# Performance work log

Measured on AMD Instinct MI355X. Metric: run time of the kernel, lower is better.

Reference implementation:

```python
import jax, jax.numpy as jnp
import numpy as np

B, D, OUT = 8192, 1024, 256
H1, H2 = 8, 4
EPS = 1e-5


def setup_inputs() -> dict:
    key = jax.random.key(0)
    ks = jax.random.split(key, 8)
    sc = lambda k, shape: jax.random.normal(k, shape, jnp.float32) * 0.05
    return {
        "x": jax.random.normal(ks[0], (B, D), jnp.float32),
        "W1": sc(ks[1], (D, H1, 1)),      # D diagonal blocks of the masked Linear(D -> 8D)
        "b1": sc(ks[2], (D * H1,)),
        "g1": jnp.ones((D * H1,), jnp.float32),
        "be1": jnp.zeros((D * H1,), jnp.float32),
        "W2": sc(ks[3], (D, H2, H1)),     # D diagonal blocks of the masked Linear(8D -> 4D)
        "b2": sc(ks[4], (D * H2,)),
        "g2": jnp.ones((D * H2,), jnp.float32),
        "be2": jnp.zeros((D * H2,), jnp.float32),
        "Wfc": sc(ks[5], (OUT, D * H2)),
        "bfc": sc(ks[6], (OUT,)),
    }


def _batchnorm(h, g, b):
    # BatchNorm1d in training mode: per-channel batch mean, biased variance
    mu = h.mean(axis=0)
    var = h.var(axis=0)  # ddof=0 (biased), matching torch normalization
    return g * (h - mu) * jax.lax.rsqrt(var + EPS) + b


def reference(x, W1, b1, g1, be1, W2, b2, g2, be2, Wfc, bfc):
    n = x.shape[0]
    # layer 1: per-feature (1 -> H1) block GEMM == masked dense Linear
    h = jnp.einsum("bdi,doi->bdo", x[:, :, None], W1).reshape(n, D * H1)
    h = jax.nn.relu(_batchnorm(h + b1, g1, be1))
    # layer 2: per-feature (H1 -> H2) block GEMM
    h = jnp.einsum("bdi,doi->bdo", h.reshape(n, D, H1), W2).reshape(n, D * H2)
    h = jax.nn.relu(_batchnorm(h + b2, g2, be2))
    # dense output head
    return h @ Wfc.T + bfc
```

## Files before the change

kernel.cpp:

```cpp
#include <hip/hip_runtime.h>

#define EPSV 1e-5f

typedef short bf16x8 __attribute__((ext_vector_type(8)));
typedef float f32x4 __attribute__((ext_vector_type(4)));

static __device__ __forceinline__ unsigned short f2b(float f) {
  union { float f; unsigned u; } v; v.f = f;
  return (unsigned short)((v.u + 0x7fffu + ((v.u >> 16) & 1u)) >> 16);
}

__global__ void k_pre(const float* __restrict__ wfc, unsigned short* __restrict__ wb,
                      const float* __restrict__ x, float* __restrict__ ps1) {
  if (blockIdx.x < 512) {
    const int f = blockIdx.x * 256 + threadIdx.x;
    const int l15 = f & 15, quad = (f >> 4) & 3, nb = (f >> 6) & 15, k32b = f >> 10;
    const int n = nb * 16 + l15;
    const int k = k32b * 32 + quad * 8;
    const float4* src = (const float4*)(wfc + (size_t)n * 4096 + k);
    float4 a = src[0], b = src[1];
    ushort4 o0, o1;
    o0.x = f2b(a.x); o0.y = f2b(a.y); o0.z = f2b(a.z); o0.w = f2b(a.w);
    o1.x = f2b(b.x); o1.y = f2b(b.y); o1.z = f2b(b.z); o1.w = f2b(b.w);
    *(ushort4*)(wb + (size_t)f * 8) = o0;
    *(ushort4*)(wb + (size_t)f * 8 + 4) = o1;
  } else {
    const int blk = blockIdx.x - 512;
    const int c = threadIdx.x * 4;
    const int r0 = blk * 32;
    float4 s = {0.f,0.f,0.f,0.f}, q = {0.f,0.f,0.f,0.f};
    for (int g = 0; g < 4; ++g) {
      float4 v[8];
#pragma unroll
      for (int j = 0; j < 8; ++j)
        v[j] = *(const float4*)(x + (size_t)(r0 + g*8 + j) * 1024 + c);
#pragma unroll
      for (int j = 0; j < 8; ++j) {
        s.x += v[j].x; s.y += v[j].y; s.z += v[j].z; s.w += v[j].w;
        q.x = fmaf(v[j].x, v[j].x, q.x); q.y = fmaf(v[j].y, v[j].y, q.y);
        q.z = fmaf(v[j].z, v[j].z, q.z); q.w = fmaf(v[j].w, v[j].w, q.w);
      }
    }
    *(float4*)(ps1 + (size_t)blk * 2048 + c) = s;
    *(float4*)(ps1 + (size_t)blk * 2048 + 1024 + c) = q;
  }
}

__global__ __launch_bounds__(256) void k_fin1(const float* __restrict__ ps1,
    const float* __restrict__ W1, const float* __restrict__ g1,
    const float* __restrict__ be1, float* __restrict__ pt) {
  __shared__ float redS[8][32], redQ[8][32];
  const int t = threadIdx.x;
  const int d0 = blockIdx.x * 32;
  const int dl = t & 31, slot = t >> 5;
  float s = 0.f, q = 0.f;
  for (int u = 0; u < 32; u += 8) {
#pragma unroll
    for (int w = 0; w < 8; ++w) {
      const size_t base = (size_t)(slot * 32 + u + w) * 2048 + d0 + dl;
      s += ps1[base];
      q += ps1[base + 1024];
    }
  }
  redS[slot][dl] = s; redQ[slot][dl] = q;
  __syncthreads();
  const int dloc = t >> 3, i = t & 7;
  float xs = 0.f, xq = 0.f;
#pragma unroll
  for (int p = 0; p < 8; ++p) { xs += redS[p][dloc]; xq += redQ[p][dloc]; }
  const float inv = 1.f / 8192.f;
  const int d = d0 + dloc;
  const int c = d * 8 + i;
  float mean = xs * inv;
  float var = xq * inv - mean * mean;
  float w = W1[c];
  float s1 = g1[c] * w * rsqrtf(w * w * var + EPSV);
  float t1 = be1[c] - s1 * mean;
  pt[i * 1024 + d] = s1;
  pt[(8 + i) * 1024 + d] = t1;
}

__global__ __launch_bounds__(256) void k_stats2(const float* __restrict__ x,
    const float* __restrict__ pt, const float* __restrict__ W2,
    float* __restrict__ ps2s, float* __restrict__ ps2q) {
  __shared__ float red[8][32][8];
  const int t = threadIdx.x;
  const int dl = t & 31, slot = t >> 5;
  const int d = blockIdx.x * 32 + dl;
  float s1v[8], t1v[8], w2v[32];
#pragma unroll
  for (int i = 0; i < 8; ++i) s1v[i] = pt[i * 1024 + d];
#pragma unroll
  for (int i = 0; i < 8; ++i) t1v[i] = pt[(8 + i) * 1024 + d];
  const float4* wp = (const float4*)(W2 + (size_t)d * 32);
#pragma unroll
  for (int i = 0; i < 8; ++i) {
    float4 v = wp[i];
    w2v[i*4+0]=v.x; w2v[i*4+1]=v.y; w2v[i*4+2]=v.z; w2v[i*4+3]=v.w;
  }
  float s[4] = {0.f,0.f,0.f,0.f}, q[4] = {0.f,0.f,0.f,0.f};
  const int b0 = blockIdx.y * 256 + slot * 32;
  for (int r = 0; r < 32; r += 8) {
    float xv[8];
#pragma unroll
    for (int j = 0; j < 8; ++j)
      xv[j] = x[(size_t)(b0 + r + j) * 1024 + d];
#pragma unroll
    for (int j = 0; j < 8; ++j) {
      float a1[8];
#pragma unroll
      for (int i = 0; i < 8; ++i) a1[i] = fmaxf(fmaf(s1v[i], xv[j], t1v[i]), 0.f);
#pragma unroll
      for (int o = 0; o < 4; ++o) {
        float h = 0.f;
#pragma unroll
        for (int i = 0; i < 8; ++i) h = fmaf(a1[i], w2v[o*8+i], h);
        s[o] += h;
        q[o] = fmaf(h, h, q[o]);
      }
    }
  }
#pragma unroll
  for (int j = 0; j < 4; ++j) {
    red[slot][dl][j] = s[j];
    red[slot][dl][4+j] = q[j];
  }
  __syncthreads();
  const int d2l = t >> 3, j = t & 7;
  float v = 0.f;
#pragma unroll
  for (int p = 0; p < 8; ++p) v += red[p][d2l][j];
  const int c2 = (blockIdx.x * 32 + d2l) * 4 + (t & 3);
  if (j < 4) ps2s[(size_t)blockIdx.y * 4096 + c2] = v;
  else       ps2q[(size_t)blockIdx.y * 4096 + c2] = v;
}

__global__ void k_fin2(const float* __restrict__ W2, const float* __restrict__ g2,
                       const float* __restrict__ be2, const float* __restrict__ ps2s,
                       const float* __restrict__ ps2q, float* __restrict__ pt) {
  const int c2 = blockIdx.x * 256 + threadIdx.x;
  const int d = c2 >> 2, o = c2 & 3;
  float sm = 0.f, sq = 0.f;
#pragma unroll
  for (int b = 0; b < 32; ++b) {
    sm += ps2s[(size_t)b * 4096 + c2];
    sq += ps2q[(size_t)b * 4096 + c2];
  }
  const float inv = 1.f / 8192.f;
  float m = sm * inv;
  float var = sq * inv - m * m;
  float s2 = g2[c2] * rsqrtf(var + EPSV);
  float t2 = be2[c2] - s2 * m;
  pt[(48 + o) * 1024 + d] = t2;
#pragma unroll
  for (int i = 0; i < 8; ++i)
    pt[(16 + o * 8 + i) * 1024 + d] = W2[(size_t)d * 32 + o * 8 + i] * s2;
}

__global__ __launch_bounds__(256, 2) void k_gemm(const float* __restrict__ x,
    const float* __restrict__ pt, const unsigned short* __restrict__ wb,
    const float* __restrict__ bfc, float* __restrict__ out) {
  __shared__ __align__(16) unsigned short As[64 * 136];
  const int t = threadIdx.x;
  const int lane = t & 63;
  const int wv = t >> 6;
  const int m0 = blockIdx.x * 64;
  const int kQ = blockIdx.y;
  const int d0 = kQ * 256;
  const int quad = lane >> 4;
  const int l15 = lane & 15;
  const int dl = t & 31, bs = t >> 5;
  const int chrot = (blockIdx.x & 1) << 2;

  f32x4 acc[4][4];
#pragma unroll
  for (int mt = 0; mt < 4; ++mt)
#pragma unroll
    for (int nt = 0; nt < 4; ++nt) {
      f32x4 z = {0.f, 0.f, 0.f, 0.f};
      acc[mt][nt] = z;
    }

  for (int chi = 0; chi < 8; ++chi) {
    const int ch = (chi + chrot) & 7;
    const int d = d0 + ch * 32 + dl;
    float pv[52];
#pragma unroll
    for (int i = 0; i < 52; ++i) pv[i] = pt[i * 1024 + d];
    __syncthreads();
#pragma unroll
    for (int r = 0; r < 8; ++r) {
      const int bl = bs * 8 + r;
      float xv = x[(size_t)(m0 + bl) * 1024 + d];
      float a1[8];
#pragma unroll
      for (int i = 0; i < 8; ++i) a1[i] = fmaxf(fmaf(pv[i], xv, pv[8+i]), 0.f);
      unsigned short o4[4];
#pragma unroll
      for (int o = 0; o < 4; ++o) {
        float h = pv[48 + o];
#pragma unroll
        for (int i = 0; i < 8; ++i) h = fmaf(a1[i], pv[16 + o*8 + i], h);
        o4[o] = f2b(fmaxf(h, 0.f));
      }
      *(ushort4*)&As[bl * 136 + dl * 4] = make_ushort4(o4[0], o4[1], o4[2], o4[3]);
    }
    __syncthreads();
#pragma unroll
    for (int kk = 0; kk < 4; ++kk) {
      bf16x8 af[4];
#pragma unroll
      for (int mt = 0; mt < 4; ++mt)
        af[mt] = *(const bf16x8*)&As[(mt*16 + l15) * 136 + kk*32 + quad*8];
      const int k32b = kQ * 32 + ch * 4 + kk;
#pragma unroll
      for (int nt = 0; nt < 4; ++nt) {
        const int frag = k32b * 16 + wv * 4 + nt;
        bf16x8 bfr = *(const bf16x8*)&wb[((size_t)frag * 64 + lane) * 8];
#pragma unroll
        for (int mt = 0; mt < 4; ++mt)
          acc[mt][nt] = __builtin_amdgcn_mfma_f32_16x16x32_bf16(af[mt], bfr,
                                                                acc[mt][nt], 0, 0, 0);
      }
    }
  }
#pragma unroll
  for (int nt = 0; nt < 4; ++nt) {
    const int col = wv * 64 + nt * 16 + l15;
    const float bias = (kQ == 0) ? bfc[col] : 0.f;
#pragma unroll
    for (int mt = 0; mt < 4; ++mt) {
#pragma unroll
      for (int r = 0; r < 4; ++r) {
        const int row = m0 + mt * 16 + quad * 4 + r;
        atomicAdd(&out[(size_t)row * 256 + col], acc[mt][nt][r] + bias);
      }
    }
  }
}

extern "C" void kernel_launch(void* const* d_in, const int* in_sizes, int n_in,
                              void* d_out, int out_size, void* d_ws, size_t ws_size,
                              hipStream_t stream) {
  const float* x   = (const float*)d_in[0];
  const float* W1  = (const float*)d_in[1];
  const float* g1  = (const float*)d_in[3];
  const float* be1 = (const float*)d_in[4];
  const float* W2  = (const float*)d_in[5];
  const float* g2  = (const float*)d_in[7];
  const float* be2 = (const float*)d_in[8];
  const float* Wfc = (const float*)d_in[9];
  const float* bfc = (const float*)d_in[10];
  float* out = (float*)d_out;

  char* ws = (char*)d_ws;
  unsigned short* wb = (unsigned short*)ws;
  float* pt     = (float*)(ws + (2u << 20));
  float* shared = (float*)(ws + (2u << 20) + (256u << 10));
  float* ps1  = shared;
  float* ps2s = shared;
  float* ps2q = shared + 32 * 4096;

  hipMemsetAsync(d_out, 0, (size_t)out_size * sizeof(float), stream);

  k_pre   <<<dim3(768),    256, 0, stream>>>(Wfc, wb, x, ps1);
  k_fin1  <<<dim3(32),     256, 0, stream>>>(ps1, W1, g1, be1, pt);
  k_stats2<<<dim3(32, 32), 256, 0, stream>>>(x, pt, W2, ps2s, ps2q);
  k_fin2  <<<dim3(16),     256, 0, stream>>>(W2, g2, be2, ps2s, ps2q, pt);
  k_gemm  <<<dim3(128, 4), 256, 0, stream>>>(x, pt, wb, bfc, out);
}
```

Measured before the change: 187.0 us.

## Fuse all stages into one persistent kernel with grid-wide atomic barriers

New measurement: 410.8 us. 120% more time.

```diff
diff --git a/kernel.cpp b/kernel.cpp
--- a/kernel.cpp
+++ b/kernel.cpp
@@ -4,16 +4,47 @@
 
 typedef short bf16x8 __attribute__((ext_vector_type(8)));
 typedef float f32x4 __attribute__((ext_vector_type(4)));
+
+#define NBLK 512
 
 static __device__ __forceinline__ unsigned short f2b(float f) {
   union { float f; unsigned u; } v; v.f = f;
   return (unsigned short)((v.u + 0x7fffu + ((v.u >> 16) & 1u)) >> 16);
 }
 
-__global__ void k_pre(const float* __restrict__ wfc, unsigned short* __restrict__ wb,
-                      const float* __restrict__ x, float* __restrict__ ps1) {
-  if (blockIdx.x < 512) {
-    const int f = blockIdx.x * 256 + threadIdx.x;
+static __device__ __forceinline__ void gbar(int* bar) {
+  __syncthreads();
+  if (threadIdx.x == 0) {
+    __hip_atomic_fetch_add(bar, 1, __ATOMIC_ACQ_REL, __HIP_MEMORY_SCOPE_AGENT);
+    for (int it = 0; it < (1 << 27); ++it) {
+      if (__hip_atomic_load(bar, __ATOMIC_ACQUIRE, __HIP_MEMORY_SCOPE_AGENT) >= NBLK)
+        break;
+    }
+  }
+  __syncthreads();
+}
+
+__global__ __launch_bounds__(256, 2) void k_all(
+    const float* __restrict__ x, const float* __restrict__ W1,
+    const float* __restrict__ g1, const float* __restrict__ be1,
+    const float* __restrict__ W2, const float* __restrict__ g2,
+    const float* __restrict__ be2, const float* __restrict__ wfc,
+    const float* __restrict__ bfc, unsigned short* __restrict__ wb,
+    float* __restrict__ pt, float* __restrict__ ps1,
+    float* __restrict__ ps2s, float* __restrict__ ps2q,
+    int* __restrict__ bars, float* __restrict__ out) {
+  __shared__ __align__(16) unsigned char smem[64 * 136 * 2];
+  const int t = threadIdx.x;
+  const int blk = blockIdx.x;
+
+  {
+    const size_t gid = (size_t)blk * 256 + t;
+    float4 z4 = {0.f, 0.f, 0.f, 0.f};
+    float4* ob = (float4*)(out + gid * 16);
+#pragma unroll
+    for (int j = 0; j < 4; ++j) ob[j] = z4;
+
+    const int f = blk * 256 + t;
     const int l15 = f & 15, quad = (f >> 4) & 3, nb = (f >> 6) & 15, k32b = f >> 10;
     const int n = nb * 16 + l15;
     const int k = k32b * 32 + quad * 8;
@@ -24,216 +55,218 @@
     o1.x = f2b(b.x); o1.y = f2b(b.y); o1.z = f2b(b.z); o1.w = f2b(b.w);
     *(ushort4*)(wb + (size_t)f * 8) = o0;
     *(ushort4*)(wb + (size_t)f * 8 + 4) = o1;
-  } else {
-    const int blk = blockIdx.x - 512;
-    const int c = threadIdx.x * 4;
-    const int r0 = blk * 32;
-    float4 s = {0.f,0.f,0.f,0.f}, q = {0.f,0.f,0.f,0.f};
-    for (int g = 0; g < 4; ++g) {
-      float4 v[8];
-#pragma unroll
-      for (int j = 0; j < 8; ++j)
-        v[j] = *(const float4*)(x + (size_t)(r0 + g*8 + j) * 1024 + c);
-#pragma unroll
-      for (int j = 0; j < 8; ++j) {
-        s.x += v[j].x; s.y += v[j].y; s.z += v[j].z; s.w += v[j].w;
-        q.x = fmaf(v[j].x, v[j].x, q.x); q.y = fmaf(v[j].y, v[j].y, q.y);
-        q.z = fmaf(v[j].z, v[j].z, q.z); q.w = fmaf(v[j].w, v[j].w, q.w);
-      }
-    }
-    *(float4*)(ps1 + (size_t)blk * 2048 + c) = s;
-    *(float4*)(ps1 + (size_t)blk * 2048 + 1024 + c) = q;
-  }
-}
-
-__global__ __launch_bounds__(256) void k_fin1(const float* __restrict__ ps1,
-    const float* __restrict__ W1, const float* __restrict__ g1,
-    const float* __restrict__ be1, float* __restrict__ pt) {
-  __shared__ float redS[8][32], redQ[8][32];
-  const int t = threadIdx.x;
-  const int d0 = blockIdx.x * 32;
-  const int dl = t & 31, slot = t >> 5;
-  float s = 0.f, q = 0.f;
-  for (int u = 0; u < 32; u += 8) {
-#pragma unroll
-    for (int w = 0; w < 8; ++w) {
-      const size_t base = (size_t)(slot * 32 + u + w) * 2048 + d0 + dl;
-      s += ps1[base];
-      q += ps1[base + 1024];
-    }
-  }
-  redS[slot][dl] = s; redQ[slot][dl] = q;
-  __syncthreads();
-  const int dloc = t >> 3, i = t & 7;
-  float xs = 0.f, xq = 0.f;
-#pragma unroll
-  for (int p = 0; p < 8; ++p) { xs += redS[p][dloc]; xq += redQ[p][dloc]; }
-  const float inv = 1.f / 8192.f;
-  const int d = d0 + dloc;
-  const int c = d * 8 + i;
-  float mean = xs * inv;
-  float var = xq * inv - mean * mean;
-  float w = W1[c];
-  float s1 = g1[c] * w * rsqrtf(w * w * var + EPSV);
-  float t1 = be1[c] - s1 * mean;
-  pt[i * 1024 + d] = s1;
-  pt[(8 + i) * 1024 + d] = t1;
-}
-
-__global__ __launch_bounds__(256) void k_stats2(const float* __restrict__ x,
-    const float* __restrict__ pt, const float* __restrict__ W2,
-    float* __restrict__ ps2s, float* __restrict__ ps2q) {
-  __shared__ float red[8][32][8];
-  const int t = threadIdx.x;
-  const int dl = t & 31, slot = t >> 5;
-  const int d = blockIdx.x * 32 + dl;
-  float s1v[8], t1v[8], w2v[32];
-#pragma unroll
-  for (int i = 0; i < 8; ++i) s1v[i] = pt[i * 1024 + d];
-#pragma unroll
-  for (int i = 0; i < 8; ++i) t1v[i] = pt[(8 + i) * 1024 + d];
-  const float4* wp = (const float4*)(W2 + (size_t)d * 32);
-#pragma unroll
-  for (int i = 0; i < 8; ++i) {
-    float4 v = wp[i];
-    w2v[i*4+0]=v.x; w2v[i*4+1]=v.y; w2v[i*4+2]=v.z; w2v[i*4+3]=v.w;
-  }
-  float s[4] = {0.f,0.f,0.f,0.f}, q[4] = {0.f,0.f,0.f,0.f};
-  const int b0 = blockIdx.y * 256 + slot * 32;
-  for (int r = 0; r < 32; r += 8) {
-    float xv[8];
-#pragma unroll
-    for (int j = 0; j < 8; ++j)
-      xv[j] = x[(size_t)(b0 + r + j) * 1024 + d];
-#pragma unroll
-    for (int j = 0; j < 8; ++j) {
-      float a1[8];
-#pragma unroll
-      for (int i = 0; i < 8; ++i) a1[i] = fmaxf(fmaf(s1v[i], xv[j], t1v[i]), 0.f);
-#pragma unroll
-      for (int o = 0; o < 4; ++o) {
-        float h = 0.f;
-#pragma unroll
-        for (int i = 0; i < 8; ++i) h = fmaf(a1[i], w2v[o*8+i], h);
-        s[o] += h;
-        q[o] = fmaf(h, h, q[o]);
-      }
-    }
-  }
-#pragma unroll
-  for (int j = 0; j < 4; ++j) {
-    red[slot][dl][j] = s[j];
-    red[slot][dl][4+j] = q[j];
-  }
-  __syncthreads();
-  const int d2l = t >> 3, j = t & 7;
-  float v = 0.f;
-#pragma unroll
-  for (int p = 0; p < 8; ++p) v += red[p][d2l][j];
-  const int c2 = (blockIdx.x * 32 + d2l) * 4 + (t & 3);
-  if (j < 4) ps2s[(size_t)blockIdx.y * 4096 + c2] = v;
-  else       ps2q[(size_t)blockIdx.y * 4096 + c2] = v;
-}
-
-__global__ void k_fin2(const float* __restrict__ W2, const float* __restrict__ g2,
-                       const float* __restrict__ be2, const float* __restrict__ ps2s,
-                       const float* __restrict__ ps2q, float* __restrict__ pt) {
-  const int c2 = blockIdx.x * 256 + threadIdx.x;
-  const int d = c2 >> 2, o = c2 & 3;
-  float sm = 0.f, sq = 0.f;
-#pragma unroll
-  for (int b = 0; b < 32; ++b) {
-    sm += ps2s[(size_t)b * 4096 + c2];
-    sq += ps2q[(size_t)b * 4096 + c2];
-  }
-  const float inv = 1.f / 8192.f;
-  float m = sm * inv;
-  float var = sq * inv - m * m;
-  float s2 = g2[c2] * rsqrtf(var + EPSV);
-  float t2 = be2[c2] - s2 * m;
-  pt[(48 + o) * 1024 + d] = t2;
-#pragma unroll
-  for (int i = 0; i < 8; ++i)
-    pt[(16 + o * 8 + i) * 1024 + d] = W2[(size_t)d * 32 + o * 8 + i] * s2;
-}
-
-__global__ __launch_bounds__(256, 2) void k_gemm(const float* __restrict__ x,
-    const float* __restrict__ pt, const unsigned short* __restrict__ wb,
-    const float* __restrict__ bfc, float* __restrict__ out) {
-  __shared__ __align__(16) unsigned short As[64 * 136];
-  const int t = threadIdx.x;
-  const int lane = t & 63;
-  const int wv = t >> 6;
-  const int m0 = blockIdx.x * 64;
-  const int kQ = blockIdx.y;
-  const int d0 = kQ * 256;
-  const int quad = lane >> 4;
-  const int l15 = lane & 15;
-  const int dl = t & 31, bs = t >> 5;
-  const int chrot = (blockIdx.x & 1) << 2;
-
-  f32x4 acc[4][4];
-#pragma unroll
-  for (int mt = 0; mt < 4; ++mt)
+
+    if (blk < 256) {
+      const int c = t * 4;
+      const int r0 = blk * 32;
+      float4 s = {0.f,0.f,0.f,0.f}, q = {0.f,0.f,0.f,0.f};
+      for (int g = 0; g < 4; ++g) {
+        float4 v[8];
+#pragma unroll
+        for (int j = 0; j < 8; ++j)
+          v[j] = *(const float4*)(x + (size_t)(r0 + g*8 + j) * 1024 + c);
+#pragma unroll
+        for (int j = 0; j < 8; ++j) {
+          s.x += v[j].x; s.y += v[j].y; s.z += v[j].z; s.w += v[j].w;
+          q.x = fmaf(v[j].x, v[j].x, q.x); q.y = fmaf(v[j].y, v[j].y, q.y);
+          q.z = fmaf(v[j].z, v[j].z, q.z); q.w = fmaf(v[j].w, v[j].w, q.w);
+        }
+      }
+      *(float4*)(ps1 + (size_t)blk * 2048 + c) = s;
+      *(float4*)(ps1 + (size_t)blk * 2048 + 1024 + c) = q;
+    }
+  }
+  gbar(&bars[0]);
+
+  if (blk < 32) {
+    float (*redS)[32] = (float (*)[32])smem;
+    float (*redQ)[32] = (float (*)[32])(smem + 8 * 32 * 4);
+    const int d0 = blk * 32;
+    const int dl = t & 31, slot = t >> 5;
+    float s = 0.f, q = 0.f;
+    for (int u = 0; u < 32; u += 8) {
+#pragma unroll
+      for (int w = 0; w < 8; ++w) {
+        const size_t base = (size_t)(slot * 32 + u + w) * 2048 + d0 + dl;
+        s += ps1[base];
+        q += ps1[base + 1024];
+      }
+    }
+    redS[slot][dl] = s; redQ[slot][dl] = q;
+    __syncthreads();
+    const int dloc = t >> 3, i = t & 7;
+    float xs = 0.f, xq = 0.f;
+#pragma unroll
+    for (int p = 0; p < 8; ++p) { xs += redS[p][dloc]; xq += redQ[p][dloc]; }
+    const float inv = 1.f / 8192.f;
+    const int d = d0 + dloc;
+    const int c = d * 8 + i;
+    float mean = xs * inv;
+    float var = xq * inv - mean * mean;
+    float w = W1[c];
+    float s1 = g1[c] * w * rsqrtf(w * w * var + EPSV);
+    float t1 = be1[c] - s1 * mean;
+    pt[i * 1024 + d] = s1;
+    pt[(8 + i) * 1024 + d] = t1;
+  }
+  gbar(&bars[1]);
+
+  {
+    float (*red)[32][8] = (float (*)[32][8])smem;
+    const int dl = t & 31, slot = t >> 5;
+#pragma unroll
+    for (int it = 0; it < 2; ++it) {
+      const int tile = blk * 2 + it;
+      const int dgrp = tile & 31, bgrp = tile >> 5;
+      const int d = dgrp * 32 + dl;
+      float s1v[8], t1v[8], w2v[32];
+#pragma unroll
+      for (int i = 0; i < 8; ++i) s1v[i] = pt[i * 1024 + d];
+#pragma unroll
+      for (int i = 0; i < 8; ++i) t1v[i] = pt[(8 + i) * 1024 + d];
+      const float4* wp = (const float4*)(W2 + (size_t)d * 32);
+#pragma unroll
+      for (int i = 0; i < 8; ++i) {
+        float4 v = wp[i];
+        w2v[i*4+0]=v.x; w2v[i*4+1]=v.y; w2v[i*4+2]=v.z; w2v[i*4+3]=v.w;
+      }
+      float s[4] = {0.f,0.f,0.f,0.f}, q[4] = {0.f,0.f,0.f,0.f};
+      const int b0 = bgrp * 256 + slot * 32;
+      for (int r = 0; r < 32; r += 8) {
+        float xv[8];
+#pragma unroll
+        for (int j = 0; j < 8; ++j)
+          xv[j] = x[(size_t)(b0 + r + j) * 1024 + d];
+#pragma unroll
+        for (int j = 0; j < 8; ++j) {
+          float a1[8];
+#pragma unroll
+          for (int i = 0; i < 8; ++i) a1[i] = fmaxf(fmaf(s1v[i], xv[j], t1v[i]), 0.f);
+#pragma unroll
+          for (int o = 0; o < 4; ++o) {
+            float h = 0.f;
+#pragma unroll
+            for (int i = 0; i < 8; ++i) h = fmaf(a1[i], w2v[o*8+i], h);
+            s[o] += h;
+            q[o] = fmaf(h, h, q[o]);
+          }
+        }
+      }
+      __syncthreads();
+#pragma unroll
+      for (int j = 0; j < 4; ++j) {
+        red[slot][dl][j] = s[j];
+        red[slot][dl][4+j] = q[j];
+      }
+      __syncthreads();
+      const int d2l = t >> 3, j = t & 7;
+      float v = 0.f;
+#pragma unroll
+      for (int p = 0; p < 8; ++p) v += red[p][d2l][j];
+      const int c2 = (dgrp * 32 + d2l) * 4 + (t & 3);
+      if (j < 4) ps2s[(size_t)bgrp * 4096 + c2] = v;
+      else       ps2q[(size_t)bgrp * 4096 + c2] = v;
+    }
+  }
+  gbar(&bars[2]);
+
+  if (blk < 16) {
+    const int c2 = blk * 256 + t;
+    const int d = c2 >> 2, o = c2 & 3;
+    float sm = 0.f, sq = 0.f;
+#pragma unroll
+    for (int b = 0; b < 32; ++b) {
+      sm += ps2s[(size_t)b * 4096 + c2];
+      sq += ps2q[(size_t)b * 4096 + c2];
+    }
+    const float inv = 1.f / 8192.f;
+    float m = sm * inv;
+    float var = sq * inv - m * m;
+    float s2 = g2[c2] * rsqrtf(var + EPSV);
+    float t2 = be2[c2] - s2 * m;
+    pt[(48 + o) * 1024 + d] = t2;
+#pragma unroll
+    for (int i = 0; i < 8; ++i)
+      pt[(16 + o * 8 + i) * 1024 + d] = W2[(size_t)d * 32 + o * 8 + i] * s2;
+  }
+  gbar(&bars[3]);
+
+  {
+    unsigned short* As = (unsigned short*)smem;
+    const int lane = t & 63;
+    const int wv = t >> 6;
+    const int mt0 = blk & 127;
+    const int kQ = blk >> 7;
+    const int m0 = mt0 * 64;
+    const int d0 = kQ * 256;
+    const int quad = lane >> 4;
+    const int l15 = lane & 15;
+    const int dl = t & 31, bs = t >> 5;
+    const int chrot = (mt0 & 1) << 2;
+
+    f32x4 acc[4][4];
+#pragma unroll
+    for (int mt = 0; mt < 4; ++mt)
+#pragma unroll
+      for (int nt = 0; nt < 4; ++nt) {
+        f32x4 z = {0.f, 0.f, 0.f, 0.f};
+        acc[mt][nt] = z;
+      }
+
+    for (int chi = 0; chi < 8; ++chi) {
+      const int ch = (chi + chrot) & 7;
+      const int d = d0 + ch * 32 + dl;
+      float pv[52];
+#pragma unroll
+      for (int i = 0; i < 52; ++i) pv[i] = pt[i * 1024 + d];
+      __syncthreads();
+#pragma unroll
+      for (int r = 0; r < 8; ++r) {
+        const int bl = bs * 8 + r;
+        float xv = x[(size_t)(m0 + bl) * 1024 + d];
+        float a1[8];
+#pragma unroll
+        for (int i = 0; i < 8; ++i) a1[i] = fmaxf(fmaf(pv[i], xv, pv[8+i]), 0.f);
+        unsigned short o4[4];
+#pragma unroll
+        for (int o = 0; o < 4; ++o) {
+          float h = pv[48 + o];
+#pragma unroll
+          for (int i = 0; i < 8; ++i) h = fmaf(a1[i], pv[16 + o*8 + i], h);
+          o4[o] = f2b(fmaxf(h, 0.f));
+        }
+        *(ushort4*)&As[bl * 136 + dl * 4] = make_ushort4(o4[0], o4[1], o4[2], o4[3]);
+      }
+      __syncthreads();
+#pragma unroll
+      for (int kk = 0; kk < 4; ++kk) {
+        bf16x8 af[4];
+#pragma unroll
+        for (int mt = 0; mt < 4; ++mt)
+          af[mt] = *(const bf16x8*)&As[(mt*16 + l15) * 136 + kk*32 + quad*8];
+        const int k32b = kQ * 32 + ch * 4 + kk;
+#pragma unroll
+        for (int nt = 0; nt < 4; ++nt) {
+          const int frag = k32b * 16 + wv * 4 + nt;
+          bf16x8 bfr = *(const bf16x8*)&wb[((size_t)frag * 64 + lane) * 8];
+#pragma unroll
+          for (int mt = 0; mt < 4; ++mt)
+            acc[mt][nt] = __builtin_amdgcn_mfma_f32_16x16x32_bf16(af[mt], bfr,
+                                                                  acc[mt][nt], 0, 0, 0);
+        }
+      }
+    }
 #pragma unroll
     for (int nt = 0; nt < 4; ++nt) {
-      f32x4 z = {0.f, 0.f, 0.f, 0.f};
-      acc[mt][nt] = z;
-    }
-
-  for (int chi = 0; chi < 8; ++chi) {
-    const int ch = (chi + chrot) & 7;
-    const int d = d0 + ch * 32 + dl;
-    float pv[52];
-#pragma unroll
-    for (int i = 0; i < 52; ++i) pv[i] = pt[i * 1024 + d];
-    __syncthreads();
-#pragma unroll
-    for (int r = 0; r < 8; ++r) {
-      const int bl = bs * 8 + r;
-      float xv = x[(size_t)(m0 + bl) * 1024 + d];
-      float a1[8];
-#pragma unroll
-      for (int i = 0; i < 8; ++i) a1[i] = fmaxf(fmaf(pv[i], xv, pv[8+i]), 0.f);
-      unsigned short o4[4];
-#pragma unroll
-      for (int o = 0; o < 4; ++o) {
-        float h = pv[48 + o];
-#pragma unroll
-        for (int i = 0; i < 8; ++i) h = fmaf(a1[i], pv[16 + o*8 + i], h);
-        o4[o] = f2b(fmaxf(h, 0.f));
-      }
-      *(ushort4*)&As[bl * 136 + dl * 4] = make_ushort4(o4[0], o4[1], o4[2], o4[3]);
-    }
-    __syncthreads();
-#pragma unroll
-    for (int kk = 0; kk < 4; ++kk) {
-      bf16x8 af[4];
-#pragma unroll
-      for (int mt = 0; mt < 4; ++mt)
-        af[mt] = *(const bf16x8*)&As[(mt*16 + l15) * 136 + kk*32 + quad*8];
-      const int k32b = kQ * 32 + ch * 4 + kk;
-#pragma unroll
-      for (int nt = 0; nt < 4; ++nt) {
-        const int frag = k32b * 16 + wv * 4 + nt;
-        bf16x8 bfr = *(const bf16x8*)&wb[((size_t)frag * 64 + lane) * 8];
-#pragma unroll
-        for (int mt = 0; mt < 4; ++mt)
-          acc[mt][nt] = __builtin_amdgcn_mfma_f32_16x16x32_bf16(af[mt], bfr,
-                                                                acc[mt][nt], 0, 0, 0);
-      }
-    }
-  }
-#pragma unroll
-  for (int nt = 0; nt < 4; ++nt) {
-    const int col = wv * 64 + nt * 16 + l15;
-    const float bias = (kQ == 0) ? bfc[col] : 0.f;
-#pragma unroll
-    for (int mt = 0; mt < 4; ++mt) {
-#pragma unroll
-      for (int r = 0; r < 4; ++r) {
-        const int row = m0 + mt * 16 + quad * 4 + r;
-        atomicAdd(&out[(size_t)row * 256 + col], acc[mt][nt][r] + bias);
+      const int col = wv * 64 + nt * 16 + l15;
+      const float bias = (kQ == 0) ? bfc[col] : 0.f;
+#pragma unroll
+      for (int mt = 0; mt < 4; ++mt) {
+#pragma unroll
+        for (int r = 0; r < 4; ++r) {
+          const int row = m0 + mt * 16 + quad * 4 + r;
+          atomicAdd(&out[(size_t)row * 256 + col], acc[mt][nt][r] + bias);
+        }
       }
     }
   }
@@ -255,17 +288,15 @@
 
   char* ws = (char*)d_ws;
   unsigned short* wb = (unsigned short*)ws;
-  float* pt     = (float*)(ws + (2u << 20));
-  float* shared = (float*)(ws + (2u << 20) + (256u << 10));
-  float* ps1  = shared;
-  float* ps2s = shared;
-  float* ps2q = shared + 32 * 4096;
-
-  hipMemsetAsync(d_out, 0, (size_t)out_size * sizeof(float), stream);
-
-  k_pre   <<<dim3(768),    256, 0, stream>>>(Wfc, wb, x, ps1);
-  k_fin1  <<<dim3(32),     256, 0, stream>>>(ps1, W1, g1, be1, pt);
-  k_stats2<<<dim3(32, 32), 256, 0, stream>>>(x, pt, W2, ps2s, ps2q);
-  k_fin2  <<<dim3(16),     256, 0, stream>>>(W2, g2, be2, ps2s, ps2q, pt);
-  k_gemm  <<<dim3(128, 4), 256, 0, stream>>>(x, pt, wb, bfc, out);
+  float* pt   = (float*)(ws + (2u << 20));
+  float* ps1  = (float*)(ws + (2u << 20) + (256u << 10));
+  float* ps2s = ps1;
+  float* ps2q = ps1 + (512u << 10) / 4;
+  int*   bars = (int*)(ws + (4u << 20) + (256u << 10));
+
+  hipMemsetAsync(bars, 0, 4 * sizeof(int), stream);
+
+  k_all<<<dim3(NBLK), dim3(256), 0, stream>>>(
+      x, W1, g1, be1, W2, g2, be2, Wfc, bfc,
+      wb, pt, ps1, ps2s, ps2q, bars, out);
 }
```

## Fuse BN finalize kernels into consumers and drop the output memset

Applied to the files above, without the earlier changes.

Result: slower. 227.2 us (+21.5%).

```diff
diff --git a/kernel.cpp b/kernel.cpp
--- a/kernel.cpp
+++ b/kernel.cpp
@@ -10,10 +10,18 @@
   return (unsigned short)((v.u + 0x7fffu + ((v.u >> 16) & 1u)) >> 16);
 }
 
-__global__ void k_pre(const float* __restrict__ wfc, unsigned short* __restrict__ wb,
-                      const float* __restrict__ x, float* __restrict__ ps1) {
+__global__ __launch_bounds__(256) void k_pre(const float* __restrict__ wfc,
+    unsigned short* __restrict__ wb, const float* __restrict__ x,
+    float* __restrict__ ps1, float* __restrict__ out) {
+  const int t = threadIdx.x;
   if (blockIdx.x < 512) {
-    const int f = blockIdx.x * 256 + threadIdx.x;
+    const int blk = blockIdx.x;
+    const size_t gid = (size_t)blk * 256 + t;
+    float4 z4 = {0.f, 0.f, 0.f, 0.f};
+    float4* ob = (float4*)(out + gid * 16);
+#pragma unroll
+    for (int j = 0; j < 4; ++j) ob[j] = z4;
+    const int f = blk * 256 + t;
     const int l15 = f & 15, quad = (f >> 4) & 3, nb = (f >> 6) & 15, k32b = f >> 10;
     const int n = nb * 16 + l15;
     const int k = k32b * 32 + quad * 8;
@@ -26,7 +34,7 @@
     *(ushort4*)(wb + (size_t)f * 8 + 4) = o1;
   } else {
     const int blk = blockIdx.x - 512;
-    const int c = threadIdx.x * 4;
+    const int c = t * 4;
     const int r0 = blk * 32;
     float4 s = {0.f,0.f,0.f,0.f}, q = {0.f,0.f,0.f,0.f};
     for (int g = 0; g < 4; ++g) {
@@ -46,52 +54,50 @@
   }
 }
 
-__global__ __launch_bounds__(256) void k_fin1(const float* __restrict__ ps1,
-    const float* __restrict__ W1, const float* __restrict__ g1,
-    const float* __restrict__ be1, float* __restrict__ pt) {
-  __shared__ float redS[8][32], redQ[8][32];
-  const int t = threadIdx.x;
-  const int d0 = blockIdx.x * 32;
-  const int dl = t & 31, slot = t >> 5;
-  float s = 0.f, q = 0.f;
-  for (int u = 0; u < 32; u += 8) {
-#pragma unroll
-    for (int w = 0; w < 8; ++w) {
-      const size_t base = (size_t)(slot * 32 + u + w) * 2048 + d0 + dl;
-      s += ps1[base];
-      q += ps1[base + 1024];
-    }
-  }
-  redS[slot][dl] = s; redQ[slot][dl] = q;
-  __syncthreads();
-  const int dloc = t >> 3, i = t & 7;
-  float xs = 0.f, xq = 0.f;
-#pragma unroll
-  for (int p = 0; p < 8; ++p) { xs += redS[p][dloc]; xq += redQ[p][dloc]; }
-  const float inv = 1.f / 8192.f;
-  const int d = d0 + dloc;
-  const int c = d * 8 + i;
-  float mean = xs * inv;
-  float var = xq * inv - mean * mean;
-  float w = W1[c];
-  float s1 = g1[c] * w * rsqrtf(w * w * var + EPSV);
-  float t1 = be1[c] - s1 * mean;
-  pt[i * 1024 + d] = s1;
-  pt[(8 + i) * 1024 + d] = t1;
-}
-
 __global__ __launch_bounds__(256) void k_stats2(const float* __restrict__ x,
-    const float* __restrict__ pt, const float* __restrict__ W2,
+    const float* __restrict__ ps1, const float* __restrict__ W1,
+    const float* __restrict__ g1, const float* __restrict__ be1,
+    const float* __restrict__ W2, float* __restrict__ pt,
     float* __restrict__ ps2s, float* __restrict__ ps2q) {
+  __shared__ float rs[8][32], rq[8][32];
   __shared__ float red[8][32][8];
   const int t = threadIdx.x;
   const int dl = t & 31, slot = t >> 5;
   const int d = blockIdx.x * 32 + dl;
+  {
+    float s = 0.f, q = 0.f;
+    for (int u = 0; u < 32; u += 4) {
+#pragma unroll
+      for (int w = 0; w < 4; ++w) {
+        const size_t base = (size_t)(slot + (u + w) * 8) * 2048 + d;
+        s += ps1[base];
+        q += ps1[base + 1024];
+      }
+    }
+    rs[slot][dl] = s; rq[slot][dl] = q;
+  }
+  __syncthreads();
+  float xs = 0.f, xq = 0.f;
+#pragma unroll
+  for (int p = 0; p < 8; ++p) { xs += rs[p][dl]; xq += rq[p][dl]; }
+  const float inv = 1.f / 8192.f;
+  const float mean = xs * inv;
+  const float var = xq * inv - mean * mean;
   float s1v[8], t1v[8], w2v[32];
 #pragma unroll
-  for (int i = 0; i < 8; ++i) s1v[i] = pt[i * 1024 + d];
-#pragma unroll
-  for (int i = 0; i < 8; ++i) t1v[i] = pt[(8 + i) * 1024 + d];
+  for (int i = 0; i < 8; ++i) {
+    const int c = d * 8 + i;
+    float w = W1[c];
+    s1v[i] = g1[c] * w * rsqrtf(w * w * var + EPSV);
+    t1v[i] = be1[c] - s1v[i] * mean;
+  }
+  if (blockIdx.y == 0 && slot == 0) {
+#pragma unroll
+    for (int i = 0; i < 8; ++i) {
+      pt[i * 1024 + d] = s1v[i];
+      pt[(8 + i) * 1024 + d] = t1v[i];
+    }
+  }
   const float4* wp = (const float4*)(W2 + (size_t)d * 32);
 #pragma unroll
   for (int i = 0; i < 8; ++i) {
@@ -135,42 +141,48 @@
   else       ps2q[(size_t)blockIdx.y * 4096 + c2] = v;
 }
 
-__global__ void k_fin2(const float* __restrict__ W2, const float* __restrict__ g2,
-                       const float* __restrict__ be2, const float* __restrict__ ps2s,
-                       const float* __restrict__ ps2q, float* __restrict__ pt) {
-  const int c2 = blockIdx.x * 256 + threadIdx.x;
-  const int d = c2 >> 2, o = c2 & 3;
-  float sm = 0.f, sq = 0.f;
-#pragma unroll
-  for (int b = 0; b < 32; ++b) {
-    sm += ps2s[(size_t)b * 4096 + c2];
-    sq += ps2q[(size_t)b * 4096 + c2];
-  }
-  const float inv = 1.f / 8192.f;
-  float m = sm * inv;
-  float var = sq * inv - m * m;
-  float s2 = g2[c2] * rsqrtf(var + EPSV);
-  float t2 = be2[c2] - s2 * m;
-  pt[(48 + o) * 1024 + d] = t2;
-#pragma unroll
-  for (int i = 0; i < 8; ++i)
-    pt[(16 + o * 8 + i) * 1024 + d] = W2[(size_t)d * 32 + o * 8 + i] * s2;
-}
-
-__global__ __launch_bounds__(256, 2) void k_gemm(const float* __restrict__ x,
+__global__ __launch_bounds__(256, 4) void k_gemm(const float* __restrict__ x,
     const float* __restrict__ pt, const unsigned short* __restrict__ wb,
-    const float* __restrict__ bfc, float* __restrict__ out) {
+    const float* __restrict__ W2, const float* __restrict__ g2,
+    const float* __restrict__ be2, const float* __restrict__ ps2s,
+    const float* __restrict__ ps2q, const float* __restrict__ bfc,
+    float* __restrict__ out) {
   __shared__ __align__(16) unsigned short As[64 * 136];
+  __shared__ float prm[128 * 37];
   const int t = threadIdx.x;
   const int lane = t & 63;
   const int wv = t >> 6;
-  const int m0 = blockIdx.x * 64;
+  const int mt0 = blockIdx.x;
   const int kQ = blockIdx.y;
-  const int d0 = kQ * 256;
+  const int m0 = mt0 * 64;
   const int quad = lane >> 4;
   const int l15 = lane & 15;
   const int dl = t & 31, bs = t >> 5;
-  const int chrot = (blockIdx.x & 1) << 2;
+  const int chrot = mt0 & 3;
+
+#pragma unroll
+  for (int rr = 0; rr < 2; ++rr) {
+    const int c2l = rr * 256 + t;
+    const int c2 = kQ * 512 + c2l;
+    float sm = 0.f, sq = 0.f;
+#pragma unroll
+    for (int p = 0; p < 32; ++p) {
+      sm += ps2s[(size_t)p * 4096 + c2];
+      sq += ps2q[(size_t)p * 4096 + c2];
+    }
+    const float inv = 1.f / 8192.f;
+    float m = sm * inv;
+    float var = sq * inv - m * m;
+    float s2 = g2[c2] * rsqrtf(var + EPSV);
+    float t2 = be2[c2] - s2 * m;
+    const int dloc = c2l >> 2, o = c2l & 3;
+    prm[dloc * 37 + 32 + o] = t2;
+#pragma unroll
+    for (int i = 0; i < 8; ++i)
+      prm[dloc * 37 + o * 8 + i] =
+          W2[(size_t)(kQ * 128 + dloc) * 32 + o * 8 + i] * s2;
+  }
+  __syncthreads();
 
   f32x4 acc[4][4];
 #pragma unroll
@@ -181,12 +193,17 @@
       acc[mt][nt] = z;
     }
 
-  for (int chi = 0; chi < 8; ++chi) {
-    const int ch = (chi + chrot) & 7;
-    const int d = d0 + ch * 32 + dl;
-    float pv[52];
-#pragma unroll
-    for (int i = 0; i < 52; ++i) pv[i] = pt[i * 1024 + d];
+  for (int chi = 0; chi < 4; ++chi) {
+    const int ch = (chi + chrot) & 3;
+    const int dloc0 = ch * 32 + dl;
+    const int d = kQ * 128 + dloc0;
+    float pv[16], w2s[32], t2c[4];
+#pragma unroll
+    for (int i = 0; i < 16; ++i) pv[i] = pt[i * 1024 + d];
+#pragma unroll
+    for (int j = 0; j < 32; ++j) w2s[j] = prm[dloc0 * 37 + j];
+#pragma unroll
+    for (int o = 0; o < 4; ++o) t2c[o] = prm[dloc0 * 37 + 32 + o];
     __syncthreads();
 #pragma unroll
     for (int r = 0; r < 8; ++r) {
@@ -198,9 +215,9 @@
       unsigned short o4[4];
 #pragma unroll
       for (int o = 0; o < 4; ++o) {
-        float h = pv[48 + o];
-#pragma unroll
-        for (int i = 0; i < 8; ++i) h = fmaf(a1[i], pv[16 + o*8 + i], h);
+        float h = t2c[o];
+#pragma unroll
+        for (int i = 0; i < 8; ++i) h = fmaf(a1[i], w2s[o*8+i], h);
         o4[o] = f2b(fmaxf(h, 0.f));
       }
       *(ushort4*)&As[bl * 136 + dl * 4] = make_ushort4(o4[0], o4[1], o4[2], o4[3]);
@@ -212,7 +229,7 @@
 #pragma unroll
       for (int mt = 0; mt < 4; ++mt)
         af[mt] = *(const bf16x8*)&As[(mt*16 + l15) * 136 + kk*32 + quad*8];
-      const int k32b = kQ * 32 + ch * 4 + kk;
+      const int k32b = kQ * 16 + ch * 4 + kk;
 #pragma unroll
       for (int nt = 0; nt < 4; ++nt) {
         const int frag = k32b * 16 + wv * 4 + nt;
@@ -255,17 +272,13 @@
 
   char* ws = (char*)d_ws;
   unsigned short* wb = (unsigned short*)ws;
-  float* pt     = (float*)(ws + (2u << 20));
-  float* shared = (float*)(ws + (2u << 20) + (256u << 10));
-  float* ps1  = shared;
-  float* ps2s = shared;
-  float* ps2q = shared + 32 * 4096;
-
-  hipMemsetAsync(d_out, 0, (size_t)out_size * sizeof(float), stream);
-
-  k_pre   <<<dim3(768),    256, 0, stream>>>(Wfc, wb, x, ps1);
-  k_fin1  <<<dim3(32),     256, 0, stream>>>(ps1, W1, g1, be1, pt);
-  k_stats2<<<dim3(32, 32), 256, 0, stream>>>(x, pt, W2, ps2s, ps2q);
-  k_fin2  <<<dim3(16),     256, 0, stream>>>(W2, g2, be2, ps2s, ps2q, pt);
-  k_gemm  <<<dim3(128, 4), 256, 0, stream>>>(x, pt, wb, bfc, out);
-}
+  float* pt   = (float*)(ws + (2u << 20));
+  float* ps1  = (float*)(ws + (2u << 20) + (256u << 10));
+  float* ps2s = (float*)(ws + (4u << 20) + (256u << 10));
+  float* ps2q = (float*)(ws + (4u << 20) + (768u << 10));
+
+  k_pre   <<<dim3(768),    256, 0, stream>>>(Wfc, wb, x, ps1, out);
+  k_stats2<<<dim3(32, 32), 256, 0, stream>>>(x, ps1, W1, g1, be1, W2, pt, ps2s, ps2q);
+  k_gemm  <<<dim3(128, 8), 256, 0, stream>>>(x, pt, wb, W2, g2, be2, ps2s, ps2q,
+                                             bfc, out);
+}
```
